# Performance work log

Measured on AMD Instinct MI355X. Metric: run time of the kernel, lower is better.

Reference implementation:

```python
import jax, jax.numpy as jnp
import numpy as np

NUM_HEADS = 16
CHUNK = 128  # module's chunk_size; softmax is computed PER key-chunk (not globally) as in the source


def setup_inputs() -> dict:
    key = jax.random.key(0)
    ks = jax.random.split(key, 6)
    B, N, C = 2, 2048, 1024
    s = 0.02
    return {
        "x": jax.random.normal(ks[0], (B, N, C), dtype=jnp.float32),
        "Wq": jax.random.normal(ks[1], (C, C), dtype=jnp.float32) * s,
        "Wk": jax.random.normal(ks[2], (C, C), dtype=jnp.float32) * s,
        "Wv": jax.random.normal(ks[3], (C, C), dtype=jnp.float32) * s,
        "Wp": jax.random.normal(ks[4], (C, C), dtype=jnp.float32) * s,
        "bp": jnp.zeros((C,), dtype=jnp.float32),
    }


def reference(x, Wq, Wk, Wv, Wp, bp):
    B, N, C = x.shape
    H = NUM_HEADS
    D = C // H
    scale = jnp.asarray(D, x.dtype) ** -0.5
    # projections (no qkv bias)
    q = (x @ Wq).reshape(B, N, H, D).transpose(0, 2, 1, 3)  # [B,H,N,D]
    k = (x @ Wk).reshape(B, N, H, D).transpose(0, 2, 1, 3)
    v = (x @ Wv).reshape(B, N, H, D).transpose(0, 2, 1, 3)
    # split keys/values into chunks of CHUNK along sequence
    nk = N // CHUNK
    kc = k.reshape(B, H, nk, CHUNK, D)
    vc = v.reshape(B, H, nk, CHUNK, D)
    # scores per key chunk: [B,H,N,nk,CHUNK]
    scores = jnp.einsum('bhnd,bhkcd->bhnkc', q, kc) * scale
    # NOTE: faithful to the source, softmax normalizes within EACH key chunk only
    attn = jax.nn.softmax(scores, axis=-1)
    # accumulate over all key chunks (the += in the torch loop)
    out = jnp.einsum('bhnkc,bhkcd->bhnd', attn, vc)  # [B,H,N,D]
    out = out.transpose(0, 2, 1, 3).reshape(B, N, C)
    return out @ Wp + bp
```

## Files before the change

kernel.cpp:

```cpp
#include <hip/hip_runtime.h>
#include <hip/hip_bf16.h>


typedef __attribute__((ext_vector_type(4))) float f32x4;
typedef __attribute__((ext_vector_type(8))) short short8;

union U4S8 { uint4 u; short8 s; };

static __device__ __forceinline__ unsigned short f2bfu(float f) {
    union { __hip_bfloat16 b; unsigned short u; } cv;
    cv.b = __float2bfloat16(f);
    return cv.u;
}
static __device__ __forceinline__ __hip_bfloat16 f2bf(float f) {
    return __float2bfloat16(f);
}
static __device__ __forceinline__ unsigned int packbf(float a, float b) {
    return (unsigned int)f2bfu(a) | ((unsigned int)f2bfu(b) << 16);
}


__global__ void conv_x_kernel(const float* __restrict__ x, __hip_bfloat16* __restrict__ xb) {
    int i = blockIdx.x * 256 + threadIdx.x;
    float4 v = ((const float4*)x)[i];
    ushort4 o;
    o.x = f2bfu(v.x); o.y = f2bfu(v.y); o.z = f2bfu(v.z); o.w = f2bfu(v.w);
    ((ushort4*)xb)[i] = o;
}

__global__ void conv_wt_kernel(const float* __restrict__ w0, const float* __restrict__ w1,
                               const float* __restrict__ w2, const float* __restrict__ w3,
                               __hip_bfloat16* __restrict__ wt) {
    __shared__ float tile[32][33];
    const float* W = (blockIdx.z == 0) ? w0 : (blockIdx.z == 1) ? w1 : (blockIdx.z == 2) ? w2 : w3;
    __hip_bfloat16* out = wt + (size_t)blockIdx.z * 1048576;
    const int tx = threadIdx.x, ty = threadIdx.y;
    const int r0 = blockIdx.y * 32, c0 = blockIdx.x * 32;
    for (int j = 0; j < 4; ++j)
        tile[ty + j * 8][tx] = W[(size_t)(r0 + ty + j * 8) * 1024 + c0 + tx];
    __syncthreads();
    for (int j = 0; j < 4; ++j)
        out[(size_t)(c0 + ty + j * 8) * 1024 + r0 + tx] = f2bf(tile[tx][ty + j * 8]);
}

__global__ __launch_bounds__(256) void gemm_qkv_kernel(
    const __hip_bfloat16* __restrict__ A, const __hip_bfloat16* __restrict__ WT,
    __hip_bfloat16* __restrict__ q_ws, __hip_bfloat16* __restrict__ k_ws,
    __hip_bfloat16* __restrict__ vT_ws) {
    const int t = threadIdx.x;
    const int lane = t & 63, w = t >> 6;
    const int quad = lane >> 4, l16 = lane & 15;
    const int wm = w >> 1, wn = w & 1;
    const int n0 = blockIdx.x * 128, m0 = blockIdx.y * 128;
    const int z = blockIdx.z;
    const __hip_bfloat16* Bt = WT + (size_t)z * 1048576;

    __shared__ __hip_bfloat16 As[128 * 48];
    __shared__ __hip_bfloat16 Bs[128 * 48];

    f32x4 acc[4][4];
    const f32x4 z4 = {0.f, 0.f, 0.f, 0.f};
    for (int i = 0; i < 4; ++i)
        for (int j = 0; j < 4; ++j) acc[i][j] = z4;

    for (int kk = 0; kk < 32; ++kk) {
        const int k0 = kk * 32;
        __syncthreads();
        for (int it = 0; it < 2; ++it) {
            int idx = it * 256 + t;
            int r = idx >> 2, sg = idx & 3;
            uint4 av = *(const uint4*)(A + (size_t)(m0 + r) * 1024 + k0 + sg * 8);
            *(uint4*)(As + r * 48 + sg * 8) = av;
            uint4 bv = *(const uint4*)(Bt + (size_t)(n0 + r) * 1024 + k0 + sg * 8);
            *(uint4*)(Bs + r * 48 + sg * 8) = bv;
        }
        __syncthreads();
        short8 af[4], bf[4];
        for (int i = 0; i < 4; ++i)
            af[i] = *(const short8*)(As + (wm * 64 + i * 16 + l16) * 48 + quad * 8);
        for (int j = 0; j < 4; ++j)
            bf[j] = *(const short8*)(Bs + (wn * 64 + j * 16 + l16) * 48 + quad * 8);
        for (int i = 0; i < 4; ++i)
            for (int j = 0; j < 4; ++j)
                acc[i][j] = __builtin_amdgcn_mfma_f32_16x16x32_bf16(af[i], bf[j], acc[i][j], 0, 0, 0);
    }

    const int r0 = m0 + wm * 64, c0 = n0 + wn * 64;
    if (z < 2) {
        const float sc = (z == 0) ? 0.18033688f : 1.0f;
        __hip_bfloat16* dst = (z == 0) ? q_ws : k_ws;
        for (int i = 0; i < 4; ++i) {
            int rowb = r0 + i * 16 + quad * 4;
            for (int j = 0; j < 4; ++j) {
                int col = c0 + j * 16 + l16;
                for (int rg = 0; rg < 4; ++rg)
                    dst[(size_t)(rowb + rg) * 1024 + col] = f2bf(acc[i][j][rg] * sc);
            }
        }
    } else {
        int b = r0 >> 11;
        for (int i = 0; i < 4; ++i) {
            int n_ = (r0 + i * 16 + quad * 4) & 2047;
            int nb = n_ & ~127;
            int c = n_ & 127;
            int vcol = (c & ~31) | (((c >> 2) & 3) << 3) | (((c >> 4) & 1) << 2);
            for (int j = 0; j < 4; ++j) {
                int col = c0 + j * 16 + l16;
                int h = col >> 6, d = col & 63;
                ushort4 o;
                o.x = f2bfu(acc[i][j][0]); o.y = f2bfu(acc[i][j][1]);
                o.z = f2bfu(acc[i][j][2]); o.w = f2bfu(acc[i][j][3]);
                *(ushort4*)(vT_ws + (size_t)((b * 16 + h) * 64 + d) * 2048 + nb + vcol) = o;
            }
        }
    }
}

__global__ __launch_bounds__(256) void gemm_final_kernel(
    const __hip_bfloat16* __restrict__ A, const __hip_bfloat16* __restrict__ Bt,
    float* __restrict__ outF, const float* __restrict__ bias) {
    const int t = threadIdx.x;
    const int lane = t & 63, w = t >> 6;
    const int quad = lane >> 4, l16 = lane & 15;
    const int n0 = blockIdx.x * 128, m0 = blockIdx.y * 64;

    __shared__ __hip_bfloat16 As[64 * 48];
    __shared__ __hip_bfloat16 Bs[128 * 48];

    f32x4 acc[4][2];
    const f32x4 z4 = {0.f, 0.f, 0.f, 0.f};
    for (int i = 0; i < 4; ++i)
        for (int j = 0; j < 2; ++j) acc[i][j] = z4;

    for (int kk = 0; kk < 32; ++kk) {
        const int k0 = kk * 32;
        __syncthreads();
        {
            int r = t >> 2, sg = t & 3;
            uint4 av = *(const uint4*)(A + (size_t)(m0 + r) * 1024 + k0 + sg * 8);
            *(uint4*)(As + r * 48 + sg * 8) = av;
        }
        for (int it = 0; it < 2; ++it) {
            int idx = it * 256 + t;
            int r = idx >> 2, sg = idx & 3;
            uint4 bv = *(const uint4*)(Bt + (size_t)(n0 + r) * 1024 + k0 + sg * 8);
            *(uint4*)(Bs + r * 48 + sg * 8) = bv;
        }
        __syncthreads();
        short8 af[4], bf[2];
        for (int i = 0; i < 4; ++i)
            af[i] = *(const short8*)(As + (i * 16 + l16) * 48 + quad * 8);
        for (int j = 0; j < 2; ++j)
            bf[j] = *(const short8*)(Bs + (w * 32 + j * 16 + l16) * 48 + quad * 8);
        for (int i = 0; i < 4; ++i)
            for (int j = 0; j < 2; ++j)
                acc[i][j] = __builtin_amdgcn_mfma_f32_16x16x32_bf16(af[i], bf[j], acc[i][j], 0, 0, 0);
    }

    for (int i = 0; i < 4; ++i) {
        int rowb = m0 + i * 16 + quad * 4;
        for (int j = 0; j < 2; ++j) {
            int col = n0 + w * 32 + j * 16 + l16;
            float bv = bias[col];
            for (int rg = 0; rg < 4; ++rg)
                outF[(size_t)(rowb + rg) * 1024 + col] = acc[i][j][rg] + bv;
        }
    }
}

__global__ __launch_bounds__(256, 2) void attn_kernel(
    const __hip_bfloat16* __restrict__ q_ws, const __hip_bfloat16* __restrict__ k_ws,
    const __hip_bfloat16* __restrict__ vT_ws, __hip_bfloat16* __restrict__ attn_ws) {
    const int t = threadIdx.x, lane = t & 63, w = t >> 6;
    const int quad = lane >> 4, l16 = lane & 15;
    const int qt = blockIdx.x;
    const int bh = blockIdx.y;
    const int b = bh >> 4, h = bh & 15;
    const int q0 = qt * 128;

    __shared__ __align__(16) char smem[71680];

    short8 qf[2][2];
#pragma unroll
    for (int mt = 0; mt < 2; ++mt)
#pragma unroll
        for (int kt = 0; kt < 2; ++kt)
            qf[mt][kt] = *(const short8*)(q_ws + (size_t)(b * 2048 + q0 + w * 32 + mt * 16 + l16) * 1024 + h * 64 + kt * 32 + quad * 8);

    const f32x4 z4 = {0.f, 0.f, 0.f, 0.f};
    f32x4 O[2][4];
#pragma unroll
    for (int mt = 0; mt < 2; ++mt)
#pragma unroll
        for (int dt = 0; dt < 4; ++dt) O[mt][dt] = z4;

    {
        __hip_bfloat16* Ksb = (__hip_bfloat16*)(smem);
        __hip_bfloat16* Vtb = (__hip_bfloat16*)(smem + 18432);
#pragma unroll
        for (int it = 0; it < 4; ++it) {
            int idx = it * 256 + t;
            int r = idx >> 3, sg = idx & 7;
            uint4 v = *(const uint4*)(k_ws + (size_t)(b * 2048 + r) * 1024 + h * 64 + sg * 8);
            *(uint4*)(Ksb + r * 72 + sg * 8) = v;
        }
#pragma unroll
        for (int it = 0; it < 4; ++it) {
            int idx = it * 256 + t;
            int d = idx >> 4, sg = idx & 15;
            uint4 v = *(const uint4*)(vT_ws + (size_t)(bh * 64 + d) * 2048 + sg * 8);
            *(uint4*)(Vtb + d * 136 + sg * 8) = v;
        }
    }
    __syncthreads();

    for (int ck = 0; ck < 16; ++ck) {
        const int cur = ck & 1;
        __hip_bfloat16* Ks = (__hip_bfloat16*)(smem + cur * 35840);
        __hip_bfloat16* Vt = (__hip_bfloat16*)(smem + cur * 35840 + 18432);

        if (ck + 1 < 16) {
            __hip_bfloat16* Ksn = (__hip_bfloat16*)(smem + (cur ^ 1) * 35840);
            __hip_bfloat16* Vtn = (__hip_bfloat16*)(smem + (cur ^ 1) * 35840 + 18432);
            const int nk0 = (ck + 1) * 128;
#pragma unroll
            for (int it = 0; it < 4; ++it) {
                int idx = it * 256 + t;
                int r = idx >> 3, sg = idx & 7;
                uint4 v = *(const uint4*)(k_ws + (size_t)(b * 2048 + nk0 + r) * 1024 + h * 64 + sg * 8);
                *(uint4*)(Ksn + r * 72 + sg * 8) = v;
            }
#pragma unroll
            for (int it = 0; it < 4; ++it) {
                int idx = it * 256 + t;
                int d = idx >> 4, sg = idx & 15;
                uint4 v = *(const uint4*)(vT_ws + (size_t)(bh * 64 + d) * 2048 + nk0 + sg * 8);
                *(uint4*)(Vtn + d * 136 + sg * 8) = v;
            }
        }

        f32x4 s[2][8];
#pragma unroll
        for (int mt = 0; mt < 2; ++mt)
#pragma unroll
            for (int i = 0; i < 8; ++i) s[mt][i] = z4;
#pragma unroll
        for (int kt = 0; kt < 2; ++kt)
#pragma unroll
            for (int i = 0; i < 8; ++i) {
                short8 kf = *(const short8*)(Ks + (i * 16 + l16) * 72 + kt * 32 + quad * 8);
                s[0][i] = __builtin_amdgcn_mfma_f32_16x16x32_bf16(kf, qf[0][kt], s[0][i], 0, 0, 0);
                s[1][i] = __builtin_amdgcn_mfma_f32_16x16x32_bf16(kf, qf[1][kt], s[1][i], 0, 0, 0);
            }

#pragma unroll
        for (int mt = 0; mt < 2; ++mt) {
            float sum = 0.f;
#pragma unroll
            for (int i = 0; i < 8; ++i) {
                f32x4 p;
                p[0] = __builtin_amdgcn_exp2f(s[mt][i][0]);
                p[1] = __builtin_amdgcn_exp2f(s[mt][i][1]);
                p[2] = __builtin_amdgcn_exp2f(s[mt][i][2]);
                p[3] = __builtin_amdgcn_exp2f(s[mt][i][3]);
                s[mt][i] = p;
                sum += (p[0] + p[1]) + (p[2] + p[3]);
            }
            sum += __shfl_xor(sum, 16, 64);
            sum += __shfl_xor(sum, 32, 64);
            const float inv = 1.0f / sum;
#pragma unroll
            for (int i = 0; i < 8; ++i) {
                s[mt][i][0] *= inv; s[mt][i][1] *= inv;
                s[mt][i][2] *= inv; s[mt][i][3] *= inv;
            }
        }

#pragma unroll
        for (int kt = 0; kt < 4; ++kt) {
            U4S8 bfr[2];
#pragma unroll
            for (int mt = 0; mt < 2; ++mt) {
                bfr[mt].u.x = packbf(s[mt][2 * kt][0], s[mt][2 * kt][1]);
                bfr[mt].u.y = packbf(s[mt][2 * kt][2], s[mt][2 * kt][3]);
                bfr[mt].u.z = packbf(s[mt][2 * kt + 1][0], s[mt][2 * kt + 1][1]);
                bfr[mt].u.w = packbf(s[mt][2 * kt + 1][2], s[mt][2 * kt + 1][3]);
            }
#pragma unroll
            for (int dt = 0; dt < 4; ++dt) {
                short8 vf = *(const short8*)(Vt + (dt * 16 + l16) * 136 + kt * 32 + quad * 8);
                O[0][dt] = __builtin_amdgcn_mfma_f32_16x16x32_bf16(vf, bfr[0].s, O[0][dt], 0, 0, 0);
                O[1][dt] = __builtin_amdgcn_mfma_f32_16x16x32_bf16(vf, bfr[1].s, O[1][dt], 0, 0, 0);
            }
        }
        __syncthreads();
    }

    __hip_bfloat16* T = (__hip_bfloat16*)smem;
#pragma unroll
    for (int mt = 0; mt < 2; ++mt)
#pragma unroll
        for (int dt = 0; dt < 4; ++dt) {
            unsigned int w0 = packbf(O[mt][dt][0], O[mt][dt][1]);
            unsigned int w1 = packbf(O[mt][dt][2], O[mt][dt][3]);
            int drow = dt * 16 + quad * 4;
            *(unsigned int*)(T + (w * 32 + mt * 16 + l16) * 72 + drow) = w0;
            *(unsigned int*)(T + (w * 32 + mt * 16 + l16) * 72 + drow + 2) = w1;
        }
    __syncthreads();
#pragma unroll
    for (int it = 0; it < 4; ++it) {
        int idx = it * 256 + t;
        int q = idx >> 3, seg = idx & 7;
        uint4 vv = *(const uint4*)(T + q * 72 + seg * 8);
        *(uint4*)(attn_ws + (size_t)(b * 2048 + q0 + q) * 1024 + h * 64 + seg * 8) = vv;
    }
}

extern "C" void kernel_launch(void* const* d_in, const int* in_sizes, int n_in,
                              void* d_out, int out_size, void* d_ws, size_t ws_size,
                              hipStream_t stream) {
    const float* x  = (const float*)d_in[0];
    const float* Wq = (const float*)d_in[1];
    const float* Wk = (const float*)d_in[2];
    const float* Wv = (const float*)d_in[3];
    const float* Wp = (const float*)d_in[4];
    const float* bp = (const float*)d_in[5];
    float* out = (float*)d_out;

    char* ws = (char*)d_ws;
    __hip_bfloat16* xb    = (__hip_bfloat16*)(ws);
    __hip_bfloat16* wT    = (__hip_bfloat16*)(ws + 8388608);
    __hip_bfloat16* q_ws  = (__hip_bfloat16*)(ws + 16777216);
    __hip_bfloat16* k_ws  = (__hip_bfloat16*)(ws + 25165824);
    __hip_bfloat16* vT_ws = (__hip_bfloat16*)(ws + 33554432);
    __hip_bfloat16* at_ws = (__hip_bfloat16*)(ws + 41943040);

    conv_x_kernel<<<4096, 256, 0, stream>>>(x, xb);
    conv_wt_kernel<<<dim3(32, 32, 4), dim3(32, 8), 0, stream>>>(Wq, Wk, Wv, Wp, wT);
    gemm_qkv_kernel<<<dim3(8, 32, 3), 256, 0, stream>>>(xb, wT, q_ws, k_ws, vT_ws);
    attn_kernel<<<dim3(16, 32), 256, 0, stream>>>(q_ws, k_ws, vT_ws, at_ws);
    gemm_final_kernel<<<dim3(8, 64), 256, 0, stream>>>(at_ws, wT + 3 * 1048576, out, bp);
}
```

Before: 195.5 us.

## Use direct global-to-LDS loads with swizzle, fuse conversion kernels, cheaper bf16 packing

Both GEMM kernels now stage A and B tiles with global_load_lds (buffer-to-LDS direct loads) into unpadded 32-wide tiles, using an XOR swizzle on the column segment to avoid LDS bank conflicts instead of padding. The x and weight conversion kernels are merged into a single launch to save one kernel launch. In attention, the softmax normalization multiply is folded into the bf16 packing step, and packing uses a cheap round-half-up bit trick with v_perm instead of full __float2bfloat16 conversion. This trades exact rounding (no NaN handling, round-half-up rather than round-to-nearest-even) for fewer instructions.

After: 184.6 us. 5.6% less time.

```diff
diff --git a/kernel.cpp b/kernel.cpp
--- a/kernel.cpp
+++ b/kernel.cpp
@@ -4,8 +4,6 @@
 
 typedef __attribute__((ext_vector_type(4))) float f32x4;
 typedef __attribute__((ext_vector_type(8))) short short8;
-
-union U4S8 { uint4 u; short8 s; };
 
 static __device__ __forceinline__ unsigned short f2bfu(float f) {
     union { __hip_bfloat16 b; unsigned short u; } cv;
@@ -15,32 +13,43 @@
 static __device__ __forceinline__ __hip_bfloat16 f2bf(float f) {
     return __float2bfloat16(f);
 }
-static __device__ __forceinline__ unsigned int packbf(float a, float b) {
-    return (unsigned int)f2bfu(a) | ((unsigned int)f2bfu(b) << 16);
-}
-
-
-__global__ void conv_x_kernel(const float* __restrict__ x, __hip_bfloat16* __restrict__ xb) {
-    int i = blockIdx.x * 256 + threadIdx.x;
-    float4 v = ((const float4*)x)[i];
-    ushort4 o;
-    o.x = f2bfu(v.x); o.y = f2bfu(v.y); o.z = f2bfu(v.z); o.w = f2bfu(v.w);
-    ((ushort4*)xb)[i] = o;
-}
-
-__global__ void conv_wt_kernel(const float* __restrict__ w0, const float* __restrict__ w1,
-                               const float* __restrict__ w2, const float* __restrict__ w3,
-                               __hip_bfloat16* __restrict__ wt) {
-    __shared__ float tile[32][33];
-    const float* W = (blockIdx.z == 0) ? w0 : (blockIdx.z == 1) ? w1 : (blockIdx.z == 2) ? w2 : w3;
-    __hip_bfloat16* out = wt + (size_t)blockIdx.z * 1048576;
-    const int tx = threadIdx.x, ty = threadIdx.y;
-    const int r0 = blockIdx.y * 32, c0 = blockIdx.x * 32;
-    for (int j = 0; j < 4; ++j)
-        tile[ty + j * 8][tx] = W[(size_t)(r0 + ty + j * 8) * 1024 + c0 + tx];
-    __syncthreads();
-    for (int j = 0; j < 4; ++j)
-        out[(size_t)(c0 + ty + j * 8) * 1024 + r0 + tx] = f2bf(tile[tx][ty + j * 8]);
+static __device__ __forceinline__ unsigned int pkrnd(float a, float b) {
+    union { float f; unsigned int u; } ua, ub;
+    ua.f = a; ub.f = b;
+    return __builtin_amdgcn_perm(ub.u + 0x8000u, ua.u + 0x8000u, 0x07060302u);
+}
+static __device__ __forceinline__ void gload_lds16(const __hip_bfloat16* g, __hip_bfloat16* l) {
+    __builtin_amdgcn_global_load_lds(
+        (const __attribute__((address_space(1))) void*)g,
+        (__attribute__((address_space(3))) void*)l, 16, 0, 0);
+}
+
+__global__ __launch_bounds__(256) void conv_fused_kernel(
+    const float* __restrict__ x, __hip_bfloat16* __restrict__ xb,
+    const float* __restrict__ w0, const float* __restrict__ w1,
+    const float* __restrict__ w2, const float* __restrict__ w3,
+    __hip_bfloat16* __restrict__ wt) {
+    const int t = threadIdx.x;
+    if (blockIdx.x < 4096) {
+        int i = blockIdx.x * 256 + t;
+        float4 v = ((const float4*)x)[i];
+        ushort4 o;
+        o.x = f2bfu(v.x); o.y = f2bfu(v.y); o.z = f2bfu(v.z); o.w = f2bfu(v.w);
+        ((ushort4*)xb)[i] = o;
+    } else {
+        __shared__ float tile[32][33];
+        int zz = blockIdx.x - 4096;
+        int z = zz >> 10, byi = (zz >> 5) & 31, bxi = zz & 31;
+        const float* W = (z == 0) ? w0 : (z == 1) ? w1 : (z == 2) ? w2 : w3;
+        __hip_bfloat16* out = wt + (size_t)z * 1048576;
+        const int tx = t & 31, ty = t >> 5;
+        const int r0 = byi * 32, c0 = bxi * 32;
+        for (int j = 0; j < 4; ++j)
+            tile[ty + j * 8][tx] = W[(size_t)(r0 + ty + j * 8) * 1024 + c0 + tx];
+        __syncthreads();
+        for (int j = 0; j < 4; ++j)
+            out[(size_t)(c0 + ty + j * 8) * 1024 + r0 + tx] = f2bf(tile[tx][ty + j * 8]);
+    }
 }
 
 __global__ __launch_bounds__(256) void gemm_qkv_kernel(
@@ -55,8 +64,16 @@
     const int z = blockIdx.z;
     const __hip_bfloat16* Bt = WT + (size_t)z * 1048576;
 
-    __shared__ __hip_bfloat16 As[128 * 48];
-    __shared__ __hip_bfloat16 Bs[128 * 48];
+    __shared__ __align__(16) __hip_bfloat16 As[128 * 32];
+    __shared__ __align__(16) __hip_bfloat16 Bs[128 * 32];
+
+    const int rS = t >> 2;
+    const int cS = ((t & 3) ^ ((t >> 3) & 3)) * 8;
+    const __hip_bfloat16* gA = A + (size_t)(m0 + rS) * 1024 + cS;
+    const __hip_bfloat16* gB = Bt + (size_t)(n0 + rS) * 1024 + cS;
+    __hip_bfloat16* lA = As + (t & 192) * 8;
+    __hip_bfloat16* lB = Bs + (t & 192) * 8;
+    const int csw = (quad ^ ((l16 >> 1) & 3)) * 8;
 
     f32x4 acc[4][4];
     const f32x4 z4 = {0.f, 0.f, 0.f, 0.f};
@@ -66,20 +83,16 @@
     for (int kk = 0; kk < 32; ++kk) {
         const int k0 = kk * 32;
         __syncthreads();
-        for (int it = 0; it < 2; ++it) {
-            int idx = it * 256 + t;
-            int r = idx >> 2, sg = idx & 3;
-            uint4 av = *(const uint4*)(A + (size_t)(m0 + r) * 1024 + k0 + sg * 8);
-            *(uint4*)(As + r * 48 + sg * 8) = av;
-            uint4 bv = *(const uint4*)(Bt + (size_t)(n0 + r) * 1024 + k0 + sg * 8);
-            *(uint4*)(Bs + r * 48 + sg * 8) = bv;
-        }
+        gload_lds16(gA + k0, lA);
+        gload_lds16(gA + 64 * 1024 + k0, lA + 256 * 8);
+        gload_lds16(gB + k0, lB);
+        gload_lds16(gB + 64 * 1024 + k0, lB + 256 * 8);
         __syncthreads();
         short8 af[4], bf[4];
         for (int i = 0; i < 4; ++i)
-            af[i] = *(const short8*)(As + (wm * 64 + i * 16 + l16) * 48 + quad * 8);
+            af[i] = *(const short8*)(As + (wm * 64 + i * 16 + l16) * 32 + csw);
         for (int j = 0; j < 4; ++j)
-            bf[j] = *(const short8*)(Bs + (wn * 64 + j * 16 + l16) * 48 + quad * 8);
+            bf[j] = *(const short8*)(Bs + (wn * 64 + j * 16 + l16) * 32 + csw);
         for (int i = 0; i < 4; ++i)
             for (int j = 0; j < 4; ++j)
                 acc[i][j] = __builtin_amdgcn_mfma_f32_16x16x32_bf16(af[i], bf[j], acc[i][j], 0, 0, 0);
@@ -124,8 +137,16 @@
     const int quad = lane >> 4, l16 = lane & 15;
     const int n0 = blockIdx.x * 128, m0 = blockIdx.y * 64;
 
-    __shared__ __hip_bfloat16 As[64 * 48];
-    __shared__ __hip_bfloat16 Bs[128 * 48];
+    __shared__ __align__(16) __hip_bfloat16 As[64 * 32];
+    __shared__ __align__(16) __hip_bfloat16 Bs[128 * 32];
+
+    const int rS = t >> 2;
+    const int cS = ((t & 3) ^ ((t >> 3) & 3)) * 8;
+    const __hip_bfloat16* gA = A + (size_t)(m0 + rS) * 1024 + cS;
+    const __hip_bfloat16* gB = Bt + (size_t)(n0 + rS) * 1024 + cS;
+    __hip_bfloat16* lA = As + (t & 192) * 8;
+    __hip_bfloat16* lB = Bs + (t & 192) * 8;
+    const int csw = (quad ^ ((l16 >> 1) & 3)) * 8;
 
     f32x4 acc[4][2];
     const f32x4 z4 = {0.f, 0.f, 0.f, 0.f};
@@ -135,23 +156,15 @@
     for (int kk = 0; kk < 32; ++kk) {
         const int k0 = kk * 32;
         __syncthreads();
-        {
-            int r = t >> 2, sg = t & 3;
-            uint4 av = *(const uint4*)(A + (size_t)(m0 + r) * 1024 + k0 + sg * 8);
-            *(uint4*)(As + r * 48 + sg * 8) = av;
-        }
-        for (int it = 0; it < 2; ++it) {
-            int idx = it * 256 + t;
-            int r = idx >> 2, sg = idx & 3;
-            uint4 bv = *(const uint4*)(Bt + (size_t)(n0 + r) * 1024 + k0 + sg * 8);
-            *(uint4*)(Bs + r * 48 + sg * 8) = bv;
-        }
+        gload_lds16(gA + k0, lA);
+        gload_lds16(gB + k0, lB);
+        gload_lds16(gB + 64 * 1024 + k0, lB + 256 * 8);
         __syncthreads();
         short8 af[4], bf[2];
         for (int i = 0; i < 4; ++i)
-            af[i] = *(const short8*)(As + (i * 16 + l16) * 48 + quad * 8);
+            af[i] = *(const short8*)(As + (i * 16 + l16) * 32 + csw);
         for (int j = 0; j < 2; ++j)
-            bf[j] = *(const short8*)(Bs + (w * 32 + j * 16 + l16) * 48 + quad * 8);
+            bf[j] = *(const short8*)(Bs + (w * 32 + j * 16 + l16) * 32 + csw);
         for (int i = 0; i < 4; ++i)
             for (int j = 0; j < 2; ++j)
                 acc[i][j] = __builtin_amdgcn_mfma_f32_16x16x32_bf16(af[i], bf[j], acc[i][j], 0, 0, 0);
@@ -253,6 +266,7 @@
                 s[1][i] = __builtin_amdgcn_mfma_f32_16x16x32_bf16(kf, qf[1][kt], s[1][i], 0, 0, 0);
             }
 
+        float inv[2];
 #pragma unroll
         for (int mt = 0; mt < 2; ++mt) {
             float sum = 0.f;
@@ -268,29 +282,26 @@
             }
             sum += __shfl_xor(sum, 16, 64);
             sum += __shfl_xor(sum, 32, 64);
-            const float inv = 1.0f / sum;
-#pragma unroll
-            for (int i = 0; i < 8; ++i) {
-                s[mt][i][0] *= inv; s[mt][i][1] *= inv;
-                s[mt][i][2] *= inv; s[mt][i][3] *= inv;
-            }
+            inv[mt] = 1.0f / sum;
         }
 
 #pragma unroll
         for (int kt = 0; kt < 4; ++kt) {
-            U4S8 bfr[2];
+            short8 bfr[2];
 #pragma unroll
             for (int mt = 0; mt < 2; ++mt) {
-                bfr[mt].u.x = packbf(s[mt][2 * kt][0], s[mt][2 * kt][1]);
-                bfr[mt].u.y = packbf(s[mt][2 * kt][2], s[mt][2 * kt][3]);
-                bfr[mt].u.z = packbf(s[mt][2 * kt + 1][0], s[mt][2 * kt + 1][1]);
-                bfr[mt].u.w = packbf(s[mt][2 * kt + 1][2], s[mt][2 * kt + 1][3]);
+                union { uint4 u; short8 s8; } bb;
+                bb.u.x = pkrnd(s[mt][2 * kt][0] * inv[mt], s[mt][2 * kt][1] * inv[mt]);
+                bb.u.y = pkrnd(s[mt][2 * kt][2] * inv[mt], s[mt][2 * kt][3] * inv[mt]);
+                bb.u.z = pkrnd(s[mt][2 * kt + 1][0] * inv[mt], s[mt][2 * kt + 1][1] * inv[mt]);
+                bb.u.w = pkrnd(s[mt][2 * kt + 1][2] * inv[mt], s[mt][2 * kt + 1][3] * inv[mt]);
+                bfr[mt] = bb.s8;
             }
 #pragma unroll
             for (int dt = 0; dt < 4; ++dt) {
                 short8 vf = *(const short8*)(Vt + (dt * 16 + l16) * 136 + kt * 32 + quad * 8);
-                O[0][dt] = __builtin_amdgcn_mfma_f32_16x16x32_bf16(vf, bfr[0].s, O[0][dt], 0, 0, 0);
-                O[1][dt] = __builtin_amdgcn_mfma_f32_16x16x32_bf16(vf, bfr[1].s, O[1][dt], 0, 0, 0);
+                O[0][dt] = __builtin_amdgcn_mfma_f32_16x16x32_bf16(vf, bfr[0], O[0][dt], 0, 0, 0);
+                O[1][dt] = __builtin_amdgcn_mfma_f32_16x16x32_bf16(vf, bfr[1], O[1][dt], 0, 0, 0);
             }
         }
         __syncthreads();
@@ -301,8 +312,8 @@
     for (int mt = 0; mt < 2; ++mt)
 #pragma unroll
         for (int dt = 0; dt < 4; ++dt) {
-            unsigned int w0 = packbf(O[mt][dt][0], O[mt][dt][1]);
-            unsigned int w1 = packbf(O[mt][dt][2], O[mt][dt][3]);
+            unsigned int w0 = pkrnd(O[mt][dt][0], O[mt][dt][1]);
+            unsigned int w1 = pkrnd(O[mt][dt][2], O[mt][dt][3]);
             int drow = dt * 16 + quad * 4;
             *(unsigned int*)(T + (w * 32 + mt * 16 + l16) * 72 + drow) = w0;
             *(unsigned int*)(T + (w * 32 + mt * 16 + l16) * 72 + drow + 2) = w1;
@@ -336,8 +347,7 @@
     __hip_bfloat16* vT_ws = (__hip_bfloat16*)(ws + 33554432);
     __hip_bfloat16* at_ws = (__hip_bfloat16*)(ws + 41943040);
 
-    conv_x_kernel<<<4096, 256, 0, stream>>>(x, xb);
-    conv_wt_kernel<<<dim3(32, 32, 4), dim3(32, 8), 0, stream>>>(Wq, Wk, Wv, Wp, wT);
+    conv_fused_kernel<<<8192, 256, 0, stream>>>(x, xb, Wq, Wk, Wv, Wp, wT);
     gemm_qkv_kernel<<<dim3(8, 32, 3), 256, 0, stream>>>(xb, wT, q_ws, k_ws, vT_ws);
     attn_kernel<<<dim3(16, 32), 256, 0, stream>>>(q_ws, k_ws, vT_ws, at_ws);
     gemm_final_kernel<<<dim3(8, 64), 256, 0, stream>>>(at_ws, wT + 3 * 1048576, out, bp);
```
